# Optimization experiments

Measured on AMD Instinct MI355X. Metric: run time of the kernel, lower is better.

Reference implementation:

```python
import jax, jax.numpy as jnp
import numpy as np


def _quant8(w):
    # Brevitas Int8 per-tensor weight quant: scale = max|w|/127, round, clip, dequant.
    s = jnp.max(jnp.abs(w)) / 127.0
    q = jnp.clip(jnp.round(w / s), -127.0, 127.0) * s
    # straight-through estimator (matches brevitas backward)
    return w + jax.lax.stop_gradient(q - w)


def _conv1d(x, w, b):
    # x: [B, Cin, L], w: [Cout, Cin, K]
    y = jax.lax.conv_general_dilated(x, w, window_strides=(1,), padding='VALID',
                                     dimension_numbers=('NCW', 'OIW', 'NCW'))
    return y + b[None, :, None]


def _maxpool2(x):
    B, C, L = x.shape
    L2 = L // 2
    return jnp.max(x[:, :, :2 * L2].reshape(B, C, L2, 2), axis=-1)


def _lrelu(x):
    return jnp.where(x > 0, x, 0.1 * x)


def setup_inputs() -> dict:
    key = jax.random.key(0)
    ks = jax.random.split(key, 13)
    B, C, L = 32768, 2, 128
    flat = 32 * 27  # 864, from tracing conv/pool stack at L=128
    d = {
        'x': jax.random.normal(ks[0], (B, C, L), dtype=jnp.float32),
        'w1': jax.random.normal(ks[1], (16, 2, 2), dtype=jnp.float32) * 0.3,
        'b1': jax.random.normal(ks[2], (16,), dtype=jnp.float32) * 0.05,
        'w2': jax.random.normal(ks[3], (16, 16, 3), dtype=jnp.float32) * 0.1,
        'b2': jax.random.normal(ks[4], (16,), dtype=jnp.float32) * 0.05,
        'w3': jax.random.normal(ks[5], (32, 16, 5), dtype=jnp.float32) * 0.1,
        'b3': jax.random.normal(ks[6], (32,), dtype=jnp.float32) * 0.05,
        'w4': jax.random.normal(ks[7], (32, 32, 5), dtype=jnp.float32) * 0.08,
        'b4': jax.random.normal(ks[8], (32,), dtype=jnp.float32) * 0.05,
        'wd': jax.random.normal(ks[9], (64, flat), dtype=jnp.float32) * 0.03,
        'bd': jax.random.normal(ks[10], (64,), dtype=jnp.float32) * 0.05,
        'wo': jax.random.normal(ks[11], (1, 64), dtype=jnp.float32) * 0.1,
        'bo': jax.random.normal(ks[12], (1,), dtype=jnp.float32) * 0.05,
    }
    return d


def reference(x, w1, b1, w2, b2, w3, b3, w4, b4, wd, bd, wo, bo):
    h = _lrelu(_conv1d(x, _quant8(w1), b1))        # [B,16,127]
    h = _lrelu(_conv1d(h, _quant8(w2), b2))        # [B,16,125]
    h = _maxpool2(h)                               # [B,16,62]
    h = _lrelu(_conv1d(h, _quant8(w3), b3))        # [B,32,58]
    h = _lrelu(_conv1d(h, _quant8(w4), b4))        # [B,32,54]
    h = _maxpool2(h)                               # [B,32,27]
    h = h.reshape(h.shape[0], -1)                  # [B,864]
    h = _lrelu(h @ _quant8(wd).T + bd)             # [B,64]
    return h @ _quant8(wo).T + bo                  # [B,1]
```

## Files before the change

### kernel.cpp

```cpp
#include <hip/hip_runtime.h>
#include <hip/hip_bf16.h>

typedef __hip_bfloat16 bf16;
typedef _Float16 h16;
typedef __attribute__((ext_vector_type(8))) _Float16 h16x8;
typedef __attribute__((ext_vector_type(4))) float f32x4;
typedef __attribute__((ext_vector_type(16))) float f32x16;

__device__ __forceinline__ float lrelu(float x) { return fmaxf(x, 0.1f * x); }
__device__ __forceinline__ float ldE(const void* p, long i, int f32) {
    return f32 ? ((const float*)p)[i] : __bfloat162float(((const bf16*)p)[i]);
}
__device__ __forceinline__ uint2 pack4(float a, float b, float c, float d) {
    union { _Float16 h[4]; uint2 u; } t;
    t.h[0] = (_Float16)a; t.h[1] = (_Float16)b; t.h[2] = (_Float16)c; t.h[3] = (_Float16)d;
    return t.u;
}
__device__ __forceinline__ unsigned umx(unsigned a, unsigned b) { return a > b ? a : b; }
#define LDS_FENCE() asm volatile("s_waitcnt lgkmcnt(0)" ::: "memory")


__device__ __forceinline__ float qv(const void* src, int idx, float sc, int f32) {
    float w = ldE(src, idx, f32);
    float q = rintf(w / sc);
    return fminf(127.f, fmaxf(-127.f, q)) * sc;
}

__device__ float block_scale(const void* src, int n, int f32, int tid, float* red) {
    unsigned m = 0;
    const uint4* p = (const uint4*)src;
    if (f32) {
        int nv = n >> 2;
        for (int i = tid; i < nv; i += 256) {
            uint4 u = p[i];
            m = umx(m, u.x & 0x7FFFFFFFu); m = umx(m, u.y & 0x7FFFFFFFu);
            m = umx(m, u.z & 0x7FFFFFFFu); m = umx(m, u.w & 0x7FFFFFFFu);
        }
        union { unsigned u; float f; } c; c.u = m;
        red[tid] = c.f;
    } else {
        int nv = n >> 3;
        for (int i = tid; i < nv; i += 256) {
            uint4 u = p[i];
            unsigned a;
            a = u.x & 0x7FFF7FFFu; m = umx(m, a >> 16); m = umx(m, a & 0xFFFFu);
            a = u.y & 0x7FFF7FFFu; m = umx(m, a >> 16); m = umx(m, a & 0xFFFFu);
            a = u.z & 0x7FFF7FFFu; m = umx(m, a >> 16); m = umx(m, a & 0xFFFFu);
            a = u.w & 0x7FFF7FFFu; m = umx(m, a >> 16); m = umx(m, a & 0xFFFFu);
        }
        union { unsigned u; float f; } c; c.u = m << 16;
        red[tid] = c.f;
    }
    __syncthreads();
    for (int s = 128; s > 0; s >>= 1) {
        if (tid < s) red[tid] = fmaxf(red[tid], red[tid + s]);
        __syncthreads();
    }
    return red[0] / 127.f;
}

__global__ void __launch_bounds__(256) prep(
    const unsigned short* __restrict__ xu,
    const void* __restrict__ w1, const void* __restrict__ w2,
    const void* __restrict__ w3, const void* __restrict__ w4,
    const void* __restrict__ wd, const void* __restrict__ wo,
    const void* __restrict__ b1, const void* __restrict__ b2,
    const void* __restrict__ b3, const void* __restrict__ b4,
    const void* __restrict__ bd, const void* __restrict__ bo,
    float* __restrict__ wsf)
{
    int tid = threadIdx.x, which = blockIdx.x;
    __shared__ float red[256];
    __shared__ int cnt;
    if (tid == 0) cnt = 0;
    __syncthreads();
    int bad = 0;
    for (int i = tid; i < 2048; i += 256) {
        int e = (xu[i] >> 7) & 0xFF;
        if (e >= 147) bad = 1;
    }
    atomicAdd(&cnt, bad);
    __syncthreads();
    const int f32 = (cnt > 4) ? 1 : 0;
    h16* wh = (h16*)(wsf + 292);

    if (which < 48) {
        float sc = block_scale(wd, 55296, f32, tid, red);
        int e1 = (which + 1) * 1152;
        for (int e = which * 1152 + tid; e < e1; e += 256) {
            int j = e & 7, l = (e >> 3) & 63, t = e >> 9;
            int mt = t / 27, c = t - mt * 27;
            int o = mt * 16 + (l & 15);
            int k = c * 32 + ((l >> 4) & 3) * 8 + j;
            int i = k >> 5, cch = k & 31;
            wh[8704 + e] = (h16)qv(wd, o * 864 + cch * 27 + i, sc, f32);
        }
    } else if (which == 48) {
        float sc = block_scale(w1, 64, f32, tid, red);
        if (tid < 64) wsf[tid] = qv(w1, tid, sc, f32);
    } else if (which == 49) {
        float sc = block_scale(w2, 768, f32, tid, red);
        for (int e = tid; e < 1024; e += 256) {
            int c = e >> 9, l = (e >> 3) & 63, j = e & 7;
            int mm = l & 15;
            int k = c * 32 + ((l >> 4) & 3) * 8 + j;
            int dk = k >> 4, ci = k & 15;
            float v = (dk < 3) ? qv(w2, (mm * 16 + ci) * 3 + dk, sc, f32) : 0.f;
            wh[0 + e] = (h16)v;
        }
    } else if (which < 52) {
        float sc = block_scale(w3, 2560, f32, tid, red);
        int e0 = (which - 50) * 1280;
        for (int e = e0 + tid; e < e0 + 1280; e += 256) {
            int c = e >> 9, l = (e >> 3) & 63, j = e & 7;
            int mm = l & 31;
            int ci = ((l >> 5) & 1) * 8 + j;
            wh[1024 + e] = (h16)qv(w3, (mm * 16 + ci) * 5 + c, sc, f32);
        }
    } else if (which < 56) {
        float sc = block_scale(w4, 5120, f32, tid, red);
        int e0 = (which - 52) * 1280;
        for (int e = e0 + tid; e < e0 + 1280; e += 256) {
            int c = e >> 9, l = (e >> 3) & 63, j = e & 7;
            int mm = l & 31;
            int k = c * 16 + ((l >> 5) & 1) * 8 + j;
            int dk = k >> 5, ci = k & 31;
            wh[3584 + e] = (h16)qv(w4, (mm * 32 + ci) * 5 + dk, sc, f32);
        }
    } else {
        float sc = block_scale(wo, 64, f32, tid, red);
        if (tid < 64) wsf[224 + tid] = qv(wo, tid, sc, f32);
        if (tid < 16)        wsf[64 + tid]        = ldE(b1, tid, f32);
        else if (tid < 32)   wsf[80 + tid - 16]   = ldE(b2, tid - 16, f32);
        else if (tid < 64)   wsf[96 + tid - 32]   = ldE(b3, tid - 32, f32);
        else if (tid < 96)   wsf[128 + tid - 64]  = ldE(b4, tid - 64, f32);
        else if (tid < 160)  wsf[160 + tid - 96]  = ldE(bd, tid - 96, f32);
        else if (tid == 160) wsf[288]             = ldE(bo, 0, f32);
        if (tid == 0) ((int*)wsf)[290] = f32;
    }
}

__global__ void __launch_bounds__(256, 3) qcnn_main(
    const void* __restrict__ x,
    const float* __restrict__ wsf,
    void* __restrict__ out)
{
    const int f32flag = ((const int*)wsf)[290];
    const float* qw1f = wsf;
    const float* fb1g = wsf + 64;
    const h16*  wh  = (const h16*)(wsf + 292);
    const h16*  F2g = wh;
    const h16*  F3g = wh + 1024;
    const h16*  F4g = wh + 3584;
    const h16*  FDg = wh + 8704;

    __shared__ __align__(16) h16 Uall[4][2112];
    __shared__ __align__(16) h16 Vall[4][2208];
    __shared__ __align__(16) h16 flatb[8][872];
    __shared__ float red[256];

    int tid  = threadIdx.x;
    int lane = tid & 63;
    int w    = __builtin_amdgcn_readfirstlane(tid >> 6);
    int n16  = lane & 15, kg16 = (lane >> 4) & 3;
    int n32  = lane & 31, kg32 = (lane >> 5) & 1;
    int o16  = kg16 * 4;
    h16* U = Uall[w];
    h16* V = Vall[w];
    long b0 = (long)blockIdx.x * 8;

    h16x8 a2[2], a3[5], a4[10];
#pragma unroll
    for (int c = 0; c < 2; ++c)  a2[c] = *(const h16x8*)&F2g[c * 512 + lane * 8];
#pragma unroll
    for (int c = 0; c < 5; ++c)  a3[c] = *(const h16x8*)&F3g[c * 512 + lane * 8];
#pragma unroll
    for (int c = 0; c < 10; ++c) a4[c] = *(const h16x8*)&F4g[c * 512 + lane * 8];
    f32x4 b2v = *(const f32x4*)&wsf[80 + o16];
    f32x16 c3i, c4i;
#pragma unroll
    for (int g = 0; g < 4; ++g) {
        f32x4 bv3 = *(const f32x4*)&wsf[96 + 8 * g + 4 * kg32];
        f32x4 bv4 = *(const f32x4*)&wsf[128 + 8 * g + 4 * kg32];
#pragma unroll
        for (int q = 0; q < 4; ++q) { c3i[4*g+q] = bv3[q]; c4i[4*g+q] = bv4[q]; }
    }

    float xl[2][2][4];
#pragma unroll
    for (int it = 0; it < 2; ++it) {
        long sb = (b0 + w * 2 + it) * 256;
#pragma unroll
        for (int ci = 0; ci < 2; ++ci) {
            int rb = ci * 128;
            xl[it][ci][0] = ldE(x, sb + rb + lane, f32flag);
            xl[it][ci][1] = ldE(x, sb + rb + lane + 1, f32flag);
            xl[it][ci][2] = ldE(x, sb + rb + 64 + lane, f32flag);
            xl[it][ci][3] = ldE(x, sb + rb + 64 + ((lane + 1) & 63), f32flag);
        }
    }

    for (int it = 0; it < 2; ++it) {
        int slot = w * 2 + it;

        LDS_FENCE();
        h16x8 ra, rbv, rc, rd;
#pragma unroll
        for (int co = 0; co < 16; ++co) {
            float w00 = qw1f[co*4+0], w01 = qw1f[co*4+1], w10 = qw1f[co*4+2], w11 = qw1f[co*4+3];
            float bb = fb1g[co];
            float v0 = bb + xl[it][0][0]*w00 + xl[it][0][1]*w01 + xl[it][1][0]*w10 + xl[it][1][1]*w11;
            float v1 = bb + xl[it][0][2]*w00 + xl[it][0][3]*w01 + xl[it][1][2]*w10 + xl[it][1][3]*w11;
            v0 = lrelu(v0); v1 = lrelu(v1);
            if (co < 8) { ra[co] = (h16)v0; rc[co] = (h16)v1; }
            else        { rbv[co-8] = (h16)v0; rd[co-8] = (h16)v1; }
        }
        *(h16x8*)&U[lane * 8]        = ra;
        *(h16x8*)&U[1056 + lane * 8] = rbv;
        if (lane < 63) {
            *(h16x8*)&U[(64 + lane) * 8]        = rc;
            *(h16x8*)&U[1056 + (64 + lane) * 8] = rd;
        }
        LDS_FENCE();

#pragma unroll
        for (int t = 0; t < 8; ++t) {
            int n = t * 16 + n16;
            f32x4 acc = b2v;
#pragma unroll
            for (int c = 0; c < 2; ++c) {
                int k0 = c * 32 + kg16 * 8;
                int dk = k0 >> 4, g = (k0 & 15) >> 3;
                h16x8 bfr = *(const h16x8*)&U[g * 1056 + (n + dk) * 8];
                acc = __builtin_amdgcn_mfma_f32_16x16x32_f16(a2[c], bfr, acc, 0, 0, 0);
            }
            if (n < 125) {
                uint2 p = pack4(lrelu(acc[0]), lrelu(acc[1]), lrelu(acc[2]), lrelu(acc[3]));
                *(uint2*)&V[(o16 >> 3) * 1008 + n * 8 + (o16 & 7)] = p;
            }
        }
        LDS_FENCE();

        if (lane < 62) {
#pragma unroll
            for (int g = 0; g < 2; ++g) {
                h16x8 pa = *(const h16x8*)&V[g * 1008 + (2 * lane) * 8];
                h16x8 pb = *(const h16x8*)&V[g * 1008 + (2 * lane + 1) * 8];
                h16x8 mm;
#pragma unroll
                for (int e = 0; e < 8; ++e) mm[e] = pa[e] > pb[e] ? pa[e] : pb[e];
                *(h16x8*)&U[g * 1056 + lane * 8] = mm;
            }
        }
        LDS_FENCE();

#pragma unroll
        for (int t = 0; t < 2; ++t) {
            int n = t * 32 + n32;
            f32x16 acc = c3i;
#pragma unroll
            for (int c = 0; c < 5; ++c) {
                h16x8 bfr = *(const h16x8*)&U[kg32 * 1056 + (n + c) * 8];
                acc = __builtin_amdgcn_mfma_f32_32x32x16_f16(a3[c], bfr, acc, 0, 0, 0);
            }
            if (n < 58) {
#pragma unroll
                for (int g = 0; g < 4; ++g) {
                    uint2 p = pack4(lrelu(acc[4*g+0]), lrelu(acc[4*g+1]),
                                    lrelu(acc[4*g+2]), lrelu(acc[4*g+3]));
                    *(uint2*)&V[g * 552 + n * 8 + 4 * kg32] = p;
                }
            }
        }
        LDS_FENCE();

#pragma unroll
        for (int t = 0; t < 2; ++t) {
            int n = t * 32 + n32;
            f32x16 acc = c4i;
#pragma unroll
            for (int c = 0; c < 10; ++c) {
                int k0 = c * 16 + kg32 * 8;
                int dk = k0 >> 5, g = (k0 >> 3) & 3;
                h16x8 bfr = *(const h16x8*)&V[g * 552 + (n + dk) * 8];
                acc = __builtin_amdgcn_mfma_f32_32x32x16_f16(a4[c], bfr, acc, 0, 0, 0);
            }
            if (n < 54) {
#pragma unroll
                for (int g = 0; g < 4; ++g) {
                    uint2 p = pack4(lrelu(acc[4*g+0]), lrelu(acc[4*g+1]),
                                    lrelu(acc[4*g+2]), lrelu(acc[4*g+3]));
                    *(uint2*)&U[g * 448 + n * 8 + 4 * kg32] = p;
                }
            }
        }
        LDS_FENCE();

        if (lane < 27) {
#pragma unroll
            for (int g = 0; g < 4; ++g) {
                h16x8 pa = *(const h16x8*)&U[g * 448 + (2 * lane) * 8];
                h16x8 pb = *(const h16x8*)&U[g * 448 + (2 * lane + 1) * 8];
                h16x8 mm;
#pragma unroll
                for (int e = 0; e < 8; ++e) mm[e] = pa[e] > pb[e] ? pa[e] : pb[e];
                *(h16x8*)&flatb[slot][(g * 27 + lane) * 8] = mm;
            }
        }
    }
    __syncthreads();

    int o0g = w * 16 + o16;
    f32x4 dacc = *(const f32x4*)&wsf[160 + o0g];
    for (int c = 0; c < 27; ++c) {
        h16x8 aw = *(const h16x8*)&FDg[((w * 27 + c) * 64 + lane) * 8];
        h16x8 bh = *(const h16x8*)&flatb[lane & 7][(kg16 * 27 + c) * 8];
        dacc = __builtin_amdgcn_mfma_f32_16x16x32_f16(aw, bh, dacc, 0, 0, 0);
    }
    f32x4 qov = *(const f32x4*)&wsf[224 + o0g];
    float part = 0.f;
#pragma unroll
    for (int q = 0; q < 4; ++q) part += lrelu(dacc[q]) * qov[q];
    red[tid] = part;
    __syncthreads();
    if (tid < 8) {
        float y = wsf[288];
#pragma unroll
        for (int g = 0; g < 16; ++g) y += red[(g >> 2) * 64 + (g & 3) * 16 + tid];
        if (f32flag) ((float*)out)[b0 + tid] = y;
        else         ((bf16*)out)[b0 + tid] = __float2bfloat16(y);
    }
}

extern "C" void kernel_launch(void* const* d_in, const int* in_sizes, int n_in,
                              void* d_out, int out_size, void* d_ws, size_t ws_size,
                              hipStream_t stream) {
    const void* x  = d_in[0];
    const void* w1 = d_in[1];
    const void* b1 = d_in[2];
    const void* w2 = d_in[3];
    const void* b2 = d_in[4];
    const void* w3 = d_in[5];
    const void* b3 = d_in[6];
    const void* w4 = d_in[7];
    const void* b4 = d_in[8];
    const void* wd = d_in[9];
    const void* bd = d_in[10];
    const void* wo = d_in[11];
    const void* bo = d_in[12];
    float* wsf = (float*)d_ws;

    int B = in_sizes[0] / 256;
    prep<<<57, 256, 0, stream>>>((const unsigned short*)x,
                                 w1, w2, w3, w4, wd, wo,
                                 b1, b2, b3, b4, bd, bo, wsf);
    qcnn_main<<<B / 8, 256, 0, stream>>>(x, wsf, d_out);
}
```

Measured before the change: 214.9 us.

## Compute conv1 with MFMA and move conv3/conv4 bias adds into epilogue

```diff
diff --git a/kernel.cpp b/kernel.cpp
--- a/kernel.cpp
+++ b/kernel.cpp
@@ -97,7 +97,12 @@
         }
     } else if (which == 48) {
         float sc = block_scale(w1, 64, f32, tid, red);
-        if (tid < 64) wsf[tid] = qv(w1, tid, sc, f32);
+        for (int e = tid; e < 512; e += 256) {
+            int l = e >> 3, j = e & 7;
+            int co = l & 15, kg = (l >> 4) & 3;
+            float v = (kg < 2 && j < 2) ? qv(w1, co * 4 + j * 2 + kg, sc, f32) : 0.f;
+            wh[64000 + e] = (h16)v;
+        }
     } else if (which == 49) {
         float sc = block_scale(w2, 768, f32, tid, red);
         for (int e = tid; e < 1024; e += 256) {
@@ -146,13 +151,12 @@
     void* __restrict__ out)
 {
     const int f32flag = ((const int*)wsf)[290];
-    const float* qw1f = wsf;
-    const float* fb1g = wsf + 64;
     const h16*  wh  = (const h16*)(wsf + 292);
     const h16*  F2g = wh;
     const h16*  F3g = wh + 1024;
     const h16*  F4g = wh + 3584;
     const h16*  FDg = wh + 8704;
+    const h16*  F1g = wh + 64000;
 
     __shared__ __align__(16) h16 Uall[4][2112];
     __shared__ __align__(16) h16 Vall[4][2208];
@@ -169,57 +173,54 @@
     h16* V = Vall[w];
     long b0 = (long)blockIdx.x * 8;
 
-    h16x8 a2[2], a3[5], a4[10];
+    h16x8 a1, a2[2], a3[5], a4[10];
+    a1 = *(const h16x8*)&F1g[lane * 8];
 #pragma unroll
     for (int c = 0; c < 2; ++c)  a2[c] = *(const h16x8*)&F2g[c * 512 + lane * 8];
 #pragma unroll
     for (int c = 0; c < 5; ++c)  a3[c] = *(const h16x8*)&F3g[c * 512 + lane * 8];
 #pragma unroll
     for (int c = 0; c < 10; ++c) a4[c] = *(const h16x8*)&F4g[c * 512 + lane * 8];
+    f32x4 b1v = *(const f32x4*)&wsf[64 + o16];
     f32x4 b2v = *(const f32x4*)&wsf[80 + o16];
-    f32x16 c3i, c4i;
-#pragma unroll
-    for (int g = 0; g < 4; ++g) {
-        f32x4 bv3 = *(const f32x4*)&wsf[96 + 8 * g + 4 * kg32];
-        f32x4 bv4 = *(const f32x4*)&wsf[128 + 8 * g + 4 * kg32];
-#pragma unroll
-        for (int q = 0; q < 4; ++q) { c3i[4*g+q] = bv3[q]; c4i[4*g+q] = bv4[q]; }
-    }
-
-    float xl[2][2][4];
-#pragma unroll
-    for (int it = 0; it < 2; ++it) {
-        long sb = (b0 + w * 2 + it) * 256;
-#pragma unroll
-        for (int ci = 0; ci < 2; ++ci) {
-            int rb = ci * 128;
-            xl[it][ci][0] = ldE(x, sb + rb + lane, f32flag);
-            xl[it][ci][1] = ldE(x, sb + rb + lane + 1, f32flag);
-            xl[it][ci][2] = ldE(x, sb + rb + 64 + lane, f32flag);
-            xl[it][ci][3] = ldE(x, sb + rb + 64 + ((lane + 1) & 63), f32flag);
-        }
-    }
+
+    const h16 hz = (h16)0.f;
+    const h16x8 zrow = {hz, hz, hz, hz, hz, hz, hz, hz};
 
     for (int it = 0; it < 2; ++it) {
         int slot = w * 2 + it;
-
-        LDS_FENCE();
-        h16x8 ra, rbv, rc, rd;
-#pragma unroll
-        for (int co = 0; co < 16; ++co) {
-            float w00 = qw1f[co*4+0], w01 = qw1f[co*4+1], w10 = qw1f[co*4+2], w11 = qw1f[co*4+3];
-            float bb = fb1g[co];
-            float v0 = bb + xl[it][0][0]*w00 + xl[it][0][1]*w01 + xl[it][1][0]*w10 + xl[it][1][1]*w11;
-            float v1 = bb + xl[it][0][2]*w00 + xl[it][0][3]*w01 + xl[it][1][2]*w10 + xl[it][1][3]*w11;
-            v0 = lrelu(v0); v1 = lrelu(v1);
-            if (co < 8) { ra[co] = (h16)v0; rc[co] = (h16)v1; }
-            else        { rbv[co-8] = (h16)v0; rd[co-8] = (h16)v1; }
-        }
-        *(h16x8*)&U[lane * 8]        = ra;
-        *(h16x8*)&U[1056 + lane * 8] = rbv;
-        if (lane < 63) {
-            *(h16x8*)&U[(64 + lane) * 8]        = rc;
-            *(h16x8*)&U[1056 + (64 + lane) * 8] = rd;
+        long sb = (b0 + slot) * 256;
+
+        LDS_FENCE();
+        {
+            float x00 = ldE(x, sb + lane, f32flag);
+            float x10 = ldE(x, sb + 128 + lane, f32flag);
+            float x01 = ldE(x, sb + 64 + lane, f32flag);
+            float x11 = ldE(x, sb + 192 + lane, f32flag);
+            h16x8 r0 = zrow, r1 = zrow;
+            r0[0] = (h16)x00; r0[1] = (h16)x10;
+            r1[0] = (h16)x01; r1[1] = (h16)x11;
+            *(h16x8*)&V[lane * 8]        = r0;
+            *(h16x8*)&V[(64 + lane) * 8] = r1;
+            if (lane < 3) *(h16x8*)&V[(128 + lane) * 8] = zrow;
+        }
+        LDS_FENCE();
+
+#pragma unroll
+        for (int t = 0; t < 8; ++t) {
+            int n = t * 16 + n16;
+            f32x4 acc = b1v;
+            h16x8 bfr = *(const h16x8*)&V[(n + kg16) * 8];
+            acc = __builtin_amdgcn_mfma_f32_16x16x32_f16(a1, bfr, acc, 0, 0, 0);
+            if (n < 127) {
+                uint2 p = pack4(lrelu(acc[0]), lrelu(acc[1]), lrelu(acc[2]), lrelu(acc[3]));
+                *(uint2*)&V[0];
+                *(uint2*)&U[(o16 >> 3) * 1056 + n * 8 + (o16 & 7)] = p;
+            }
+        }
+        if (lane < 8) {
+            int g = lane & 1, row = 127 + (lane >> 1);
+            *(uint4*)&U[g * 1056 + row * 8] = make_uint4(0, 0, 0, 0);
         }
         LDS_FENCE();
 
@@ -257,7 +258,7 @@
 #pragma unroll
         for (int t = 0; t < 2; ++t) {
             int n = t * 32 + n32;
-            f32x16 acc = c3i;
+            f32x16 acc = {0.f,0.f,0.f,0.f,0.f,0.f,0.f,0.f,0.f,0.f,0.f,0.f,0.f,0.f,0.f,0.f};
 #pragma unroll
             for (int c = 0; c < 5; ++c) {
                 h16x8 bfr = *(const h16x8*)&U[kg32 * 1056 + (n + c) * 8];
@@ -266,8 +267,10 @@
             if (n < 58) {
 #pragma unroll
                 for (int g = 0; g < 4; ++g) {
-                    uint2 p = pack4(lrelu(acc[4*g+0]), lrelu(acc[4*g+1]),
-                                    lrelu(acc[4*g+2]), lrelu(acc[4*g+3]));
+                    int r0 = 8 * g + 4 * kg32;
+                    f32x4 bv = *(const f32x4*)&wsf[96 + r0];
+                    uint2 p = pack4(lrelu(acc[4*g+0] + bv[0]), lrelu(acc[4*g+1] + bv[1]),
+                                    lrelu(acc[4*g+2] + bv[2]), lrelu(acc[4*g+3] + bv[3]));
                     *(uint2*)&V[g * 552 + n * 8 + 4 * kg32] = p;
                 }
             }
@@ -277,7 +280,7 @@
 #pragma unroll
         for (int t = 0; t < 2; ++t) {
             int n = t * 32 + n32;
-            f32x16 acc = c4i;
+            f32x16 acc = {0.f,0.f,0.f,0.f,0.f,0.f,0.f,0.f,0.f,0.f,0.f,0.f,0.f,0.f,0.f,0.f};
 #pragma unroll
             for (int c = 0; c < 10; ++c) {
                 int k0 = c * 16 + kg32 * 8;
@@ -288,8 +291,10 @@
             if (n < 54) {
 #pragma unroll
                 for (int g = 0; g < 4; ++g) {
-                    uint2 p = pack4(lrelu(acc[4*g+0]), lrelu(acc[4*g+1]),
-                                    lrelu(acc[4*g+2]), lrelu(acc[4*g+3]));
+                    int r0 = 8 * g + 4 * kg32;
+                    f32x4 bv = *(const f32x4*)&wsf[128 + r0];
+                    uint2 p = pack4(lrelu(acc[4*g+0] + bv[0]), lrelu(acc[4*g+1] + bv[1]),
+                                    lrelu(acc[4*g+2] + bv[2]), lrelu(acc[4*g+3] + bv[3]));
                     *(uint2*)&U[g * 448 + n * 8 + 4 * kg32] = p;
                 }
             }
```

After: 200.0 us. 1.07x faster.
